# Performance work log

Measured on AMD Instinct MI355X. Metric: run time of the kernel, lower is better.

Reference implementation:

```python
import jax, jax.numpy as jnp
import numpy as np

B, T, D = 256, 64, 512          # batch, seq_len, enc_input_size == dec_output_size
HE, L = 1024, 512               # enc_hidden_size, latent == con_hidden == dec_hidden
BAR, BAR_UNITS = 4, 16          # conductor bars, steps per bar (BAR*BAR_UNITS == T)


def _lstm_step(x, h, c, Wih, Whh, bih, bhh):
    # torch LSTM gate order: i, f, g, o
    g = x @ Wih.T + bih + h @ Whh.T + bhh
    i, f, gg, o = jnp.split(g, 4, axis=-1)
    c = jax.nn.sigmoid(f) * c + jax.nn.sigmoid(i) * jnp.tanh(gg)
    h = jax.nn.sigmoid(o) * jnp.tanh(c)
    return h, c


def _run_lstm_final_h(x_t, Wih, Whh, bih, bhh):
    # x_t: (T, B, D_in); returns final hidden state (B, H)
    Bb = x_t.shape[1]
    H = Whh.shape[1]
    init = (jnp.zeros((Bb, H), x_t.dtype), jnp.zeros((Bb, H), x_t.dtype))
    def step(carry, xt):
        h, c = _lstm_step(xt, carry[0], carry[1], Wih, Whh, bih, bhh)
        return (h, c), None
    (h, _), _ = jax.lax.scan(step, init, x_t)
    return h


def reference(x, eps, We_ih_f, We_hh_f, be_ih_f, be_hh_f, We_ih_b, We_hh_b, be_ih_b, be_hh_b,
              Wmu, bmu, Wstd, bstd, Wc_ih0, Wc_hh0, bc_ih0, bc_hh0, Wc_ih1, Wc_hh1, bc_ih1, bc_hh1,
              Wcl, bcl, Wd_ih0, Wd_hh0, bd_ih0, bd_hh0, Wd_ih1, Wd_hh1, bd_ih1, bd_hh1, Wlog, blog):
    x_t = jnp.transpose(x, (1, 0, 2))  # (T, B, D)
    # ---- Encoder: 1-layer bidirectional LSTM, take final hidden of each direction ----
    h_f = _run_lstm_final_h(x_t, We_ih_f, We_hh_f, be_ih_f, be_hh_f)
    h_b = _run_lstm_final_h(x_t[::-1], We_ih_b, We_hh_b, be_ih_b, be_hh_b)
    henc = jnp.concatenate([h_f, h_b], axis=-1)  # (B, 2*HE)
    mu_raw = henc @ Wmu.T + bmu
    mu = (mu_raw - mu_raw.mean(-1, keepdims=True)) / jnp.sqrt(mu_raw.var(-1, keepdims=True) + 1e-5)
    std = jax.nn.softplus(henc @ Wstd.T + bstd)
    z = mu + eps * std  # (B, L)
    # ---- Conductor: 2-layer LSTM, h0=c0=z, input is z at every bar step ----
    h0 = c0 = h1 = c1 = z
    feats = []
    for _ in range(BAR):
        h0, c0 = _lstm_step(z, h0, c0, Wc_ih0, Wc_hh0, bc_ih0, bc_hh0)
        h1, c1 = _lstm_step(h0, h1, c1, Wc_ih1, Wc_hh1, bc_ih1, bc_hh1)
        feats.append(h1)
    feat = jnp.stack(feats, axis=1) @ Wcl.T + bcl  # (B, BAR, L)
    # ---- Decoder: 2-layer LSTM, teacher-forced, hidden reset to bar embedding each bar ----
    z_t = jnp.transpose(jnp.repeat(feat, BAR_UNITS, axis=1), (1, 0, 2))  # (T, B, L)
    x_prev_t = jnp.concatenate([jnp.zeros((1, x.shape[0], D), x.dtype), x_t[:-1]], axis=0)
    reset_t = (jnp.arange(T) % BAR_UNITS) == 0
    zH = jnp.zeros((x.shape[0], L), x.dtype)
    def dec_step(carry, inp):
        hd1, cd1, hd2, cd2 = carry
        xp, zb, rs = inp
        hd1 = jnp.where(rs, zb, hd1); cd1 = jnp.where(rs, zb, cd1)
        hd2 = jnp.where(rs, zb, hd2); cd2 = jnp.where(rs, zb, cd2)
        xin = jnp.concatenate([xp, zb], axis=-1)  # (B, D+L)
        hd1, cd1 = _lstm_step(xin, hd1, cd1, Wd_ih0, Wd_hh0, bd_ih0, bd_hh0)
        hd2, cd2 = _lstm_step(hd1, hd2, cd2, Wd_ih1, Wd_hh1, bd_ih1, bd_hh1)
        logits = hd2 @ Wlog.T + blog  # temp == 1
        return (hd1, cd1, hd2, cd2), logits
    _, logits_t = jax.lax.scan(dec_step, (zH, zH, zH, zH), (x_prev_t, z_t, reset_t))
    prob = jnp.transpose(jax.nn.softmax(logits_t, axis=-1), (1, 0, 2))  # (B, T, D)
    label = jnp.argmax(prob, axis=-1).astype(jnp.float32)  # (B, T)
    return prob, mu, std, label


def setup_inputs() -> dict:
    key = jax.random.key(0)
    ks = iter(jax.random.split(key, 40))
    def w(shape, fan):
        return jax.random.normal(next(ks), shape, jnp.float32) * (1.0 / np.sqrt(fan))
    return {
        'x': jax.random.normal(next(ks), (B, T, D), jnp.float32),
        'eps': jax.random.normal(next(ks), (B, L), jnp.float32),
        'We_ih_f': w((4 * HE, D), HE), 'We_hh_f': w((4 * HE, HE), HE),
        'be_ih_f': w((4 * HE,), HE), 'be_hh_f': w((4 * HE,), HE),
        'We_ih_b': w((4 * HE, D), HE), 'We_hh_b': w((4 * HE, HE), HE),
        'be_ih_b': w((4 * HE,), HE), 'be_hh_b': w((4 * HE,), HE),
        'Wmu': w((L, 2 * HE), 2 * HE), 'bmu': w((L,), 2 * HE),
        'Wstd': w((L, 2 * HE), 2 * HE), 'bstd': w((L,), 2 * HE),
        'Wc_ih0': w((4 * L, L), L), 'Wc_hh0': w((4 * L, L), L),
        'bc_ih0': w((4 * L,), L), 'bc_hh0': w((4 * L,), L),
        'Wc_ih1': w((4 * L, L), L), 'Wc_hh1': w((4 * L, L), L),
        'bc_ih1': w((4 * L,), L), 'bc_hh1': w((4 * L,), L),
        'Wcl': w((L, L), L), 'bcl': w((L,), L),
        'Wd_ih0': w((4 * L, L + D), L), 'Wd_hh0': w((4 * L, L), L),
        'bd_ih0': w((4 * L,), L), 'bd_hh0': w((4 * L,), L),
        'Wd_ih1': w((4 * L, L), L), 'Wd_hh1': w((4 * L, L), L),
        'bd_ih1': w((4 * L,), L), 'bd_hh1': w((4 * L,), L),
        'Wlog': w((D, L), L), 'blog': w((D,), L),
    }
```

## Files before the change

### kernel.cpp

```cpp
#include <hip/hip_runtime.h>
#include <cstddef>
#include <cstdint>

static constexpr int B  = 256;
static constexpr int T  = 64;
static constexpr int D  = 512;
static constexpr int HE = 1024;
static constexpr int L  = 512;

typedef unsigned short ushort_t;
typedef __attribute__((ext_vector_type(8))) short short8;
typedef __attribute__((ext_vector_type(8))) _Float16 f16x8;
typedef __attribute__((ext_vector_type(4))) float f32x4;
typedef __attribute__((ext_vector_type(4))) unsigned short ushort4_t;

static constexpr float LO_SCALE   = 2048.0f;
static constexpr float LO_UNSCALE = 4.8828125e-4f;

__device__ __forceinline__ float sigmoidf_(float x) { return 1.0f / (1.0f + expf(-x)); }

struct hfp { ushort_t hi, lo; };
__device__ __forceinline__ hfp f16_split(float v) {
    _Float16 h = (_Float16)v;
    _Float16 l = (_Float16)((v - (float)h) * LO_SCALE);
    hfp r;
    r.hi = __builtin_bit_cast(ushort_t, h);
    r.lo = __builtin_bit_cast(ushort_t, l);
    return r;
}

__device__ __forceinline__ size_t tile_off(int m, int n, int ldt) {
    return ((size_t)(m >> 4) * ldt + (n >> 5)) * 512
         + (size_t)((((m & 15) + (((n >> 3) & 3) << 4)) << 3) + (n & 7));
}

__global__ void pack_w(const float* __restrict__ src, ushort_t* __restrict__ hi,
                       ushort_t* __restrict__ lo, int Np, int K, int H)
{
    int idx = blockIdx.x * 256 + threadIdx.x;
    int pc = K >> 2;
    if (idx >= Np * pc) return;
    int p = idx / pc, kc = (idx - p * pc) << 2;
    int srow = p;
    if (H) srow = ((p >> 4) & 3) * H + (p >> 6) * 16 + (p & 15);
    float4 v = *(const float4*)(src + (size_t)srow * K + kc);
    ushort4_t h, l;
    hfp a;
    a = f16_split(v.x); h[0] = a.hi; l[0] = a.lo;
    a = f16_split(v.y); h[1] = a.hi; l[1] = a.lo;
    a = f16_split(v.z); h[2] = a.hi; l[2] = a.lo;
    a = f16_split(v.w); h[3] = a.hi; l[3] = a.lo;
    size_t off = tile_off(p, kc, K >> 5);
    *(ushort4_t*)(hi + off) = h;
    *(ushort4_t*)(lo + off) = l;
}

__global__ void pack_bias(const float* __restrict__ b1, const float* __restrict__ b2,
                          float* __restrict__ dst, int H)
{
    int p = blockIdx.x * 256 + threadIdx.x;
    if (p >= 4 * H) return;
    int srow = ((p >> 4) & 3) * H + (p >> 6) * 16 + (p & 15);
    dst[p] = b1[srow] + b2[srow];
}

__global__ void conv_x(const float* __restrict__ x, ushort_t* __restrict__ xh,
                       ushort_t* __restrict__ xl)
{
    int idx = blockIdx.x * 256 + threadIdx.x;
    if (idx >= T * B * D / 4) return;
    int r = idx >> 7;
    int kc = (idx & 127) << 2;
    int t = r >> 8, b = r & 255;
    float4 v = *(const float4*)(x + ((size_t)b * T + t) * D + kc);
    ushort4_t h, l;
    hfp a;
    a = f16_split(v.x); h[0] = a.hi; l[0] = a.lo;
    a = f16_split(v.y); h[1] = a.hi; l[1] = a.lo;
    a = f16_split(v.z); h[2] = a.hi; l[2] = a.lo;
    a = f16_split(v.w); h[3] = a.hi; l[3] = a.lo;
    size_t off = (size_t)t * B * D + tile_off(b, kc, D >> 5);
    *(ushort4_t*)(xh + off) = h;
    *(ushort4_t*)(xl + off) = l;
}

struct Op {
    const ushort_t *Ahi, *Alo; int ldtA, kt0A;
    const ushort_t *Whi, *Wlo; int ldtW, kt0W;
    int K;
};
struct MArgs {
    Op op[3];
    const float* ci0; int ld0;
    int mode;
    const float* cin; int cinLd;
    float* cout; int coutLd;
    ushort_t *hHi, *hLo; int hLdT;
    float* out; int outLd;
    ushort_t *pHi, *pLo; int pLdT;
};

__device__ __forceinline__ f32x4 MFH(short8 a, short8 w, f32x4 c) {
    return __builtin_amdgcn_mfma_f32_16x16x32_f16(
        __builtin_bit_cast(f16x8, a), __builtin_bit_cast(f16x8, w), c, 0, 0, 0);
}

template<int TAG>
__global__ __launch_bounds__(256) void gemm_sk(MArgs ga0, MArgs ga1)
{
    __shared__ float LV[4][2][4][4][64];
    const MArgs& ga = blockIdx.z ? ga1 : ga0;
    const int tid  = threadIdx.x;
    const int lane = tid & 63;
    const int wk   = tid >> 6;
    const int m_w = blockIdx.y * 32;
    const int n_w = blockIdx.x * 64;
    const int l15 = lane & 15;

    f32x4 accH[2][4], accL[2][4];
#pragma unroll
    for (int mf = 0; mf < 2; ++mf)
#pragma unroll
        for (int j = 0; j < 4; ++j)
#pragma unroll
            for (int r = 0; r < 4; ++r) { accH[mf][j][r] = 0.0f; accL[mf][j][r] = 0.0f; }

    int NT = 0;
#pragma unroll
    for (int opi = 0; opi < 3; ++opi)
        if (ga.op[opi].Ahi && ga.op[opi].K > 0) NT += ga.op[opi].K >> 5;
    const int share = NT >> 2;
    int skip = wk * share, cnt = share;

#pragma unroll 1
    for (int opi = 0; opi < 3 && cnt > 0; ++opi) {
        const Op o = ga.op[opi];
        if (o.Ahi == nullptr || o.K <= 0) continue;
        const int NK = o.K >> 5;
        if (skip >= NK) { skip -= NK; continue; }
        const int k0 = skip;
        const int k1 = (NK - k0 < cnt) ? NK : k0 + cnt;
        cnt -= (k1 - k0);
        skip = 0;

        const ushort_t *aHp[2], *aLp[2], *wHp[4], *wLp[4];
#pragma unroll
        for (int mf = 0; mf < 2; ++mf) {
            size_t ro = ((size_t)((m_w >> 4) + mf) * o.ldtA + o.kt0A) * 512 + lane * 8;
            aHp[mf] = o.Ahi + ro; aLp[mf] = o.Alo + ro;
        }
#pragma unroll
        for (int j = 0; j < 4; ++j) {
            size_t ro = ((size_t)((n_w >> 4) + j) * o.ldtW + o.kt0W) * 512 + lane * 8;
            wHp[j] = o.Whi + ro; wLp[j] = o.Wlo + ro;
        }

        short8 A0[2], L0[2], W0[4], V0[4];
        short8 A1[2], L1[2], W1[4], V1[4];
        auto LD0 = [&](int ks) {
#pragma unroll
            for (int mf = 0; mf < 2; ++mf) {
                A0[mf] = *(const short8*)(aHp[mf] + (size_t)ks * 512);
                L0[mf] = *(const short8*)(aLp[mf] + (size_t)ks * 512);
            }
#pragma unroll
            for (int j = 0; j < 4; ++j) {
                W0[j] = *(const short8*)(wHp[j] + (size_t)ks * 512);
                V0[j] = *(const short8*)(wLp[j] + (size_t)ks * 512);
            }
        };
        auto LD1 = [&](int ks) {
#pragma unroll
            for (int mf = 0; mf < 2; ++mf) {
                A1[mf] = *(const short8*)(aHp[mf] + (size_t)ks * 512);
                L1[mf] = *(const short8*)(aLp[mf] + (size_t)ks * 512);
            }
#pragma unroll
            for (int j = 0; j < 4; ++j) {
                W1[j] = *(const short8*)(wHp[j] + (size_t)ks * 512);
                V1[j] = *(const short8*)(wLp[j] + (size_t)ks * 512);
            }
        };
        auto MM0 = [&]() {
#pragma unroll
            for (int mf = 0; mf < 2; ++mf)
#pragma unroll
                for (int j = 0; j < 4; ++j) {
                    accL[mf][j] = MFH(A0[mf], V0[j], accL[mf][j]);
                    accL[mf][j] = MFH(L0[mf], W0[j], accL[mf][j]);
                    accH[mf][j] = MFH(A0[mf], W0[j], accH[mf][j]);
                }
        };
        auto MM1 = [&]() {
#pragma unroll
            for (int mf = 0; mf < 2; ++mf)
#pragma unroll
                for (int j = 0; j < 4; ++j) {
                    accL[mf][j] = MFH(A1[mf], V1[j], accL[mf][j]);
                    accL[mf][j] = MFH(L1[mf], W1[j], accL[mf][j]);
                    accH[mf][j] = MFH(A1[mf], W1[j], accH[mf][j]);
                }
        };

        LD0(k0);
        int ks = k0;
        for (; ks + 2 < k1; ks += 2) {
            LD1(ks + 1);
            MM0();
            LD0(ks + 2);
            MM1();
        }
        if (ks + 1 < k1) { LD1(ks + 1); MM0(); MM1(); }
        else MM0();
    }

#pragma unroll
    for (int mf = 0; mf < 2; ++mf)
#pragma unroll
        for (int j = 0; j < 4; ++j)
#pragma unroll
            for (int r = 0; r < 4; ++r)
                LV[wk][mf][j][r][lane] = accH[mf][j][r] + LO_UNSCALE * accL[mf][j][r];
    __syncthreads();

    const int mf = wk >> 1;
    const int rb = (wk & 1) * 2;
#pragma unroll
    for (int rr = 0; rr < 2; ++rr) {
        const int r = rb + rr;
        float g[4];
#pragma unroll
        for (int j = 0; j < 4; ++j) {
            float s = 0.0f;
#pragma unroll
            for (int w2 = 0; w2 < 4; ++w2) s += LV[w2][mf][j][r][lane];
            if (ga.ci0) s += ga.ci0[n_w + j * 16 + l15];
            g[j] = s;
        }
        const int m = m_w + mf * 16 + (lane >> 4) * 4 + r;
        if (ga.mode == 1) {
            const int n = (n_w >> 6) * 16 + l15;
            const float cold = ga.cin[(size_t)m * ga.cinLd + n];
            const float cn = sigmoidf_(g[1]) * cold + sigmoidf_(g[0]) * tanhf(g[2]);
            const float h  = sigmoidf_(g[3]) * tanhf(cn);
            ga.cout[(size_t)m * ga.coutLd + n] = cn;
            hfp hp = f16_split(h);
            size_t off = tile_off(m, n, ga.hLdT);
            ga.hHi[off] = hp.hi;
            ga.hLo[off] = hp.lo;
        } else {
#pragma unroll
            for (int j = 0; j < 4; ++j) {
                const int p = n_w + j * 16 + l15;
                int dst = m;
                if (ga.mode == 2) dst = ((m & (B - 1)) << 6) + (m >> 8);
                if (ga.out) ga.out[(size_t)dst * ga.outLd + p] = g[j];
                if (ga.pHi) {
                    hfp vp = f16_split(g[j]);
                    size_t off = tile_off(m, p, ga.pLdT);
                    ga.pHi[off] = vp.hi;
                    ga.pLo[off] = vp.lo;
                }
            }
        }
    }
}

template<int TAG, int MF, int WM, int WN>
__global__ __launch_bounds__(WM * WN * 64) void gemm_t(MArgs ga0, MArgs ga1)
{
    const MArgs& ga = blockIdx.z ? ga1 : ga0;
    const int lane = threadIdx.x & 63;
    const int wid  = threadIdx.x >> 6;
    const int wy = wid / WN, wx = wid % WN;
    const int m_w = blockIdx.y * (WM * MF * 16) + wy * MF * 16;
    const int n_w = blockIdx.x * (WN * 64) + wx * 64;
    const int l15 = lane & 15;
    const int rB  = (lane >> 4) * 4;

    f32x4 accH[MF][4];
    f32x4 accL[MF][4];
#pragma unroll
    for (int mf = 0; mf < MF; ++mf)
#pragma unroll
        for (int j = 0; j < 4; ++j) {
            const int p = n_w + j * 16 + l15;
#pragma unroll
            for (int r = 0; r < 4; ++r) {
                float v = 0.0f;
                if (ga.ci0) v += ga.ci0[(size_t)(m_w + mf * 16 + rB + r) * ga.ld0 + p];
                accH[mf][j][r] = v;
                accL[mf][j][r] = 0.0f;
            }
        }

#pragma unroll 1
    for (int opi = 0; opi < 3; ++opi) {
        const Op o = ga.op[opi];
        if (o.Ahi == nullptr || o.K <= 0) continue;
        const ushort_t *aH[MF], *aL[MF], *wH[4], *wL[4];
#pragma unroll
        for (int mf = 0; mf < MF; ++mf) {
            size_t ro = ((size_t)((m_w >> 4) + mf) * o.ldtA + o.kt0A) * 512 + lane * 8;
            aH[mf] = o.Ahi + ro; aL[mf] = o.Alo + ro;
        }
#pragma unroll
        for (int j = 0; j < 4; ++j) {
            size_t ro = ((size_t)((n_w >> 4) + j) * o.ldtW + o.kt0W) * 512 + lane * 8;
            wH[j] = o.Whi + ro; wL[j] = o.Wlo + ro;
        }
        const int NK = o.K >> 5;

        auto LD = [&](short8* ah, short8* al, short8* wh, short8* wl, int ks) {
#pragma unroll
            for (int mf = 0; mf < MF; ++mf) {
                ah[mf] = *(const short8*)(aH[mf] + (size_t)ks * 512);
                al[mf] = *(const short8*)(aL[mf] + (size_t)ks * 512);
            }
#pragma unroll
            for (int j = 0; j < 4; ++j) {
                wh[j] = *(const short8*)(wH[j] + (size_t)ks * 512);
                wl[j] = *(const short8*)(wL[j] + (size_t)ks * 512);
            }
        };
        auto MM = [&](short8* ah, short8* al, short8* wh, short8* wl) {
#pragma unroll
            for (int mf = 0; mf < MF; ++mf)
#pragma unroll
                for (int j = 0; j < 4; ++j) {
                    accL[mf][j] = MFH(ah[mf], wl[j], accL[mf][j]);
                    accL[mf][j] = MFH(al[mf], wh[j], accL[mf][j]);
                    accH[mf][j] = MFH(ah[mf], wh[j], accH[mf][j]);
                }
        };

        short8 A0[MF], L0[MF], W0[4], V0[4];
        short8 A1[MF], L1[MF], W1[4], V1[4];
        LD(A0, L0, W0, V0, 0);
        int ks = 0;
        for (; ks + 2 < NK; ks += 2) {
            LD(A1, L1, W1, V1, ks + 1);
            MM(A0, L0, W0, V0);
            LD(A0, L0, W0, V0, ks + 2);
            MM(A1, L1, W1, V1);
        }
        LD(A1, L1, W1, V1, ks + 1);
        MM(A0, L0, W0, V0);
        MM(A1, L1, W1, V1);
    }

    if (ga.mode == 1) {
        const int n = (n_w >> 6) * 16 + l15;
#pragma unroll
        for (int mf = 0; mf < MF; ++mf)
#pragma unroll
            for (int r = 0; r < 4; ++r) {
                const int m = m_w + mf * 16 + rB + r;
                const float gi = accH[mf][0][r] + LO_UNSCALE * accL[mf][0][r];
                const float gf = accH[mf][1][r] + LO_UNSCALE * accL[mf][1][r];
                const float gg = accH[mf][2][r] + LO_UNSCALE * accL[mf][2][r];
                const float go = accH[mf][3][r] + LO_UNSCALE * accL[mf][3][r];
                const float cold = ga.cin[(size_t)m * ga.cinLd + n];
                const float cn = sigmoidf_(gf) * cold + sigmoidf_(gi) * tanhf(gg);
                const float h  = sigmoidf_(go) * tanhf(cn);
                ga.cout[(size_t)m * ga.coutLd + n] = cn;
                hfp hp = f16_split(h);
                size_t off = tile_off(m, n, ga.hLdT);
                ga.hHi[off] = hp.hi;
                ga.hLo[off] = hp.lo;
            }
    } else {
#pragma unroll
        for (int mf = 0; mf < MF; ++mf)
#pragma unroll
            for (int j = 0; j < 4; ++j) {
                const int p = n_w + j * 16 + l15;
#pragma unroll
                for (int r = 0; r < 4; ++r) {
                    const int m = m_w + mf * 16 + rB + r;
                    const float v = accH[mf][j][r] + LO_UNSCALE * accL[mf][j][r];
                    int dst = m;
                    if (ga.mode == 2) dst = ((m & (B - 1)) << 6) + (m >> 8);
                    if (ga.out) ga.out[(size_t)dst * ga.outLd + p] = v;
                    if (ga.pHi) {
                        hfp vp = f16_split(v);
                        size_t off = tile_off(m, p, ga.pLdT);
                        ga.pHi[off] = vp.hi;
                        ga.pLo[off] = vp.lo;
                    }
                }
            }
    }
}

__global__ void latent2(float* __restrict__ mu, float* __restrict__ sd,
                        const float* __restrict__ eps, float* __restrict__ c0,
                        float* __restrict__ c1, ushort_t* __restrict__ zh,
                        ushort_t* __restrict__ zl)
{
    const int b = blockIdx.x, l = threadIdx.x;
    float* mrow = mu + (size_t)b * L;
    float4 v0 = *(const float4*)(mrow + l * 4);
    float4 v1 = *(const float4*)(mrow + 256 + l * 4);
    float s = v0.x + v0.y + v0.z + v0.w + v1.x + v1.y + v1.z + v1.w;
    float q = v0.x * v0.x + v0.y * v0.y + v0.z * v0.z + v0.w * v0.w
            + v1.x * v1.x + v1.y * v1.y + v1.z * v1.z + v1.w * v1.w;
#pragma unroll
    for (int off = 32; off; off >>= 1) { s += __shfl_xor(s, off); q += __shfl_xor(q, off); }
    const float mean = s * (1.0f / 512.0f);
    const float var  = q * (1.0f / 512.0f) - mean * mean;
    const float inv  = rsqrtf(var + 1e-5f);
    v0.x = (v0.x - mean) * inv; v0.y = (v0.y - mean) * inv; v0.z = (v0.z - mean) * inv; v0.w = (v0.w - mean) * inv;
    v1.x = (v1.x - mean) * inv; v1.y = (v1.y - mean) * inv; v1.z = (v1.z - mean) * inv; v1.w = (v1.w - mean) * inv;
    *(float4*)(mrow + l * 4) = v0;
    *(float4*)(mrow + 256 + l * 4) = v1;

    float* srow = sd + (size_t)b * L;
    float4 s0 = *(const float4*)(srow + l * 4);
    float4 s1 = *(const float4*)(srow + 256 + l * 4);
    s0.x = fmaxf(s0.x, 0.0f) + log1pf(expf(-fabsf(s0.x)));
    s0.y = fmaxf(s0.y, 0.0f) + log1pf(expf(-fabsf(s0.y)));
    s0.z = fmaxf(s0.z, 0.0f) + log1pf(expf(-fabsf(s0.z)));
    s0.w = fmaxf(s0.w, 0.0f) + log1pf(expf(-fabsf(s0.w)));
    s1.x = fmaxf(s1.x, 0.0f) + log1pf(expf(-fabsf(s1.x)));
    s1.y = fmaxf(s1.y, 0.0f) + log1pf(expf(-fabsf(s1.y)));
    s1.z = fmaxf(s1.z, 0.0f) + log1pf(expf(-fabsf(s1.z)));
    s1.w = fmaxf(s1.w, 0.0f) + log1pf(expf(-fabsf(s1.w)));
    *(float4*)(srow + l * 4) = s0;
    *(float4*)(srow + 256 + l * 4) = s1;

    const float* erow = eps + (size_t)b * L;
    float4 e0 = *(const float4*)(erow + l * 4);
    float4 e1 = *(const float4*)(erow + 256 + l * 4);
    float4 z0, z1;
    z0.x = v0.x + e0.x * s0.x; z0.y = v0.y + e0.y * s0.y; z0.z = v0.z + e0.z * s0.z; z0.w = v0.w + e0.w * s0.w;
    z1.x = v1.x + e1.x * s1.x; z1.y = v1.y + e1.y * s1.y; z1.z = v1.z + e1.z * s1.z; z1.w = v1.w + e1.w * s1.w;
    *(float4*)(c0 + (size_t)b * L + l * 4) = z0;
    *(float4*)(c0 + (size_t)b * L + 256 + l * 4) = z1;
    *(float4*)(c1 + (size_t)b * L + l * 4) = z0;
    *(float4*)(c1 + (size_t)b * L + 256 + l * 4) = z1;
    ushort4_t h, lo;
    hfp a;
    a = f16_split(z0.x); h[0] = a.hi; lo[0] = a.lo;
    a = f16_split(z0.y); h[1] = a.hi; lo[1] = a.lo;
    a = f16_split(z0.z); h[2] = a.hi; lo[2] = a.lo;
    a = f16_split(z0.w); h[3] = a.hi; lo[3] = a.lo;
    size_t o0 = tile_off(b, l * 4, 16);
    *(ushort4_t*)(zh + o0) = h;
    *(ushort4_t*)(zl + o0) = lo;
    a = f16_split(z1.x); h[0] = a.hi; lo[0] = a.lo;
    a = f16_split(z1.y); h[1] = a.hi; lo[1] = a.lo;
    a = f16_split(z1.z); h[2] = a.hi; lo[2] = a.lo;
    a = f16_split(z1.w); h[3] = a.hi; lo[3] = a.lo;
    size_t o1 = tile_off(b, 256 + l * 4, 16);
    *(ushort4_t*)(zh + o1) = h;
    *(ushort4_t*)(zl + o1) = lo;
}

__global__ void softmax_all(float* __restrict__ prob, float* __restrict__ label)
{
    const int r = blockIdx.x, l = threadIdx.x;
    float* row = prob + (size_t)r * D;
    float4 x0 = *(const float4*)(row + l * 4);
    float4 x1 = *(const float4*)(row + 256 + l * 4);
    float m = x0.x; int mi = l * 4;
    { float v; int i;
      v = x0.y; i = l * 4 + 1;       if (v > m) { m = v; mi = i; }
      v = x0.z; i = l * 4 + 2;       if (v > m) { m = v; mi = i; }
      v = x0.w; i = l * 4 + 3;       if (v > m) { m = v; mi = i; }
      v = x1.x; i = 256 + l * 4;     if (v > m) { m = v; mi = i; }
      v = x1.y; i = 256 + l * 4 + 1; if (v > m) { m = v; mi = i; }
      v = x1.z; i = 256 + l * 4 + 2; if (v > m) { m = v; mi = i; }
      v = x1.w; i = 256 + l * 4 + 3; if (v > m) { m = v; mi = i; } }
#pragma unroll
    for (int off = 32; off; off >>= 1) {
        float om = __shfl_xor(m, off);
        int   oi = __shfl_xor(mi, off);
        if (om > m || (om == m && oi < mi)) { m = om; mi = oi; }
    }
    float4 e0, e1;
    e0.x = expf(x0.x - m); e0.y = expf(x0.y - m); e0.z = expf(x0.z - m); e0.w = expf(x0.w - m);
    e1.x = expf(x1.x - m); e1.y = expf(x1.y - m); e1.z = expf(x1.z - m); e1.w = expf(x1.w - m);
    float s = e0.x + e0.y + e0.z + e0.w + e1.x + e1.y + e1.z + e1.w;
#pragma unroll
    for (int off = 32; off; off >>= 1) s += __shfl_xor(s, off);
    const float inv = 1.0f / s;
    e0.x *= inv; e0.y *= inv; e0.z *= inv; e0.w *= inv;
    e1.x *= inv; e1.y *= inv; e1.z *= inv; e1.w *= inv;
    *(float4*)(row + l * 4) = e0;
    *(float4*)(row + 256 + l * 4) = e1;
    if (l == 0) label[r] = (float)mi;
}

extern "C" void kernel_launch(void* const* d_in, const int* in_sizes, int n_in,
                              void* d_out, int out_size, void* d_ws, size_t ws_size,
                              hipStream_t stream)
{
    const float* x       = (const float*)d_in[0];
    const float* eps     = (const float*)d_in[1];
    const float* We_ih_f = (const float*)d_in[2];
    const float* We_hh_f = (const float*)d_in[3];
    const float* be_ih_f = (const float*)d_in[4];
    const float* be_hh_f = (const float*)d_in[5];
    const float* We_ih_b = (const float*)d_in[6];
    const float* We_hh_b = (const float*)d_in[7];
    const float* be_ih_b = (const float*)d_in[8];
    const float* be_hh_b = (const float*)d_in[9];
    const float* Wmu     = (const float*)d_in[10];
    const float* bmu     = (const float*)d_in[11];
    const float* Wstd    = (const float*)d_in[12];
    const float* bstd    = (const float*)d_in[13];
    const float* Wc_ih0  = (const float*)d_in[14];
    const float* Wc_hh0  = (const float*)d_in[15];
    const float* bc_ih0  = (const float*)d_in[16];
    const float* bc_hh0  = (const float*)d_in[17];
    const float* Wc_ih1  = (const float*)d_in[18];
    const float* Wc_hh1  = (const float*)d_in[19];
    const float* bc_ih1  = (const float*)d_in[20];
    const float* bc_hh1  = (const float*)d_in[21];
    const float* Wcl     = (const float*)d_in[22];
    const float* bcl     = (const float*)d_in[23];
    const float* Wd_ih0  = (const float*)d_in[24];
    const float* Wd_hh0  = (const float*)d_in[25];
    const float* bd_ih0  = (const float*)d_in[26];
    const float* bd_hh0  = (const float*)d_in[27];
    const float* Wd_ih1  = (const float*)d_in[28];
    const float* Wd_hh1  = (const float*)d_in[29];
    const float* bd_ih1  = (const float*)d_in[30];
    const float* bd_hh1  = (const float*)d_in[31];
    const float* Wlog    = (const float*)d_in[32];
    const float* blog    = (const float*)d_in[33];
    (void)in_sizes; (void)n_in; (void)out_size;

    float* out      = (float*)d_out;
    float* prob_out = out;
    float* mu_out   = out + (size_t)B * T * D;
    float* std_out  = mu_out + (size_t)B * L;
    float* lab_out  = std_out + (size_t)B * L;

    char* cur = (char*)d_ws;
    auto alignup = [&]() { cur = (char*)(((uintptr_t)cur + 255) & ~(uintptr_t)255); };
    auto aU = [&](size_t elems) { alignup(); ushort_t* p = (ushort_t*)cur; cur += elems * 2; return p; };
    auto aF = [&](size_t elems) { alignup(); float* p = (float*)cur; cur += elems * 4; return p; };

    ushort_t* WefIh = aU((size_t)4*HE*D);  ushort_t* WefIl = aU((size_t)4*HE*D);
    ushort_t* WefHh = aU((size_t)4*HE*HE); ushort_t* WefHl = aU((size_t)4*HE*HE);
    ushort_t* WebIh = aU((size_t)4*HE*D);  ushort_t* WebIl = aU((size_t)4*HE*D);
    ushort_t* WebHh = aU((size_t)4*HE*HE); ushort_t* WebHl = aU((size_t)4*HE*HE);
    ushort_t* Wc0Ih = aU((size_t)4*L*L);   ushort_t* Wc0Il = aU((size_t)4*L*L);
    ushort_t* Wc0Hh = aU((size_t)4*L*L);   ushort_t* Wc0Hl = aU((size_t)4*L*L);
    ushort_t* Wc1Ih = aU((size_t)4*L*L);   ushort_t* Wc1Il = aU((size_t)4*L*L);
    ushort_t* Wc1Hh = aU((size_t)4*L*L);   ushort_t* Wc1Hl = aU((size_t)4*L*L);
    ushort_t* Wd0Ih = aU((size_t)4*L*(D+L)); ushort_t* Wd0Il = aU((size_t)4*L*(D+L));
    ushort_t* Wd0Hh = aU((size_t)4*L*L);   ushort_t* Wd0Hl = aU((size_t)4*L*L);
    ushort_t* Wd1Ih = aU((size_t)4*L*L);   ushort_t* Wd1Il = aU((size_t)4*L*L);
    ushort_t* Wd1Hh = aU((size_t)4*L*L);   ushort_t* Wd1Hl = aU((size_t)4*L*L);
    ushort_t* WmuH  = aU((size_t)L*2*HE);  ushort_t* WmuL  = aU((size_t)L*2*HE);
    ushort_t* WstdH = aU((size_t)L*2*HE);  ushort_t* WstdL = aU((size_t)L*2*HE);
    ushort_t* WclH  = aU((size_t)L*L);     ushort_t* WclL  = aU((size_t)L*L);
    ushort_t* WlogH = aU((size_t)D*L);     ushort_t* WlogL = aU((size_t)D*L);
    ushort_t* xh = aU((size_t)T*B*D);      ushort_t* xl = aU((size_t)T*B*D);
    ushort_t* hfh[2] = { aU((size_t)B*HE), aU((size_t)B*HE) };
    ushort_t* hfl[2] = { aU((size_t)B*HE), aU((size_t)B*HE) };
    ushort_t* hbh[2] = { aU((size_t)B*HE), aU((size_t)B*HE) };
    ushort_t* hbl[2] = { aU((size_t)B*HE), aU((size_t)B*HE) };
    ushort_t* zh = aU((size_t)B*L);        ushort_t* zl = aU((size_t)B*L);
    ushort_t* h0h[2] = { aU((size_t)B*L), aU((size_t)B*L) };
    ushort_t* h0l[2] = { aU((size_t)B*L), aU((size_t)B*L) };
    ushort_t* ftsH = aU((size_t)4*B*L);    ushort_t* ftsL = aU((size_t)4*B*L);
    ushort_t* featH = aU((size_t)4*B*L);   ushort_t* featL = aU((size_t)4*B*L);
    ushort_t* hd1h[2] = { aU((size_t)B*L), aU((size_t)B*L) };
    ushort_t* hd1l[2] = { aU((size_t)B*L), aU((size_t)B*L) };
    ushort_t* slabH = aU((size_t)T*B*L);   ushort_t* slabL = aU((size_t)T*B*L);
    float* cf   = aF((size_t)B*HE);
    float* cb   = aF((size_t)B*HE);
    float* zbuf = aF((size_t)B*HE);
    float* c0   = aF((size_t)B*L);
    float* c1   = aF((size_t)B*L);
    float* cd1  = aF((size_t)B*L);
    float* cd2  = aF((size_t)B*L);
    float* featF = aF((size_t)4*B*L);
    float* bEF = aF((size_t)4*HE);
    float* bEB = aF((size_t)4*HE);
    float* bC0 = aF((size_t)4*L);
    float* bC1 = aF((size_t)4*L);
    float* bD0 = aF((size_t)4*L);
    float* bD1 = aF((size_t)4*L);
    const size_t need = (size_t)(cur - (char*)d_ws);
    if (need > ws_size) return;

    auto PK = [&](const float* s, ushort_t* h, ushort_t* l, int Np, int K, int H) {
        int tot = Np * (K >> 2);
        pack_w<<<(tot + 255) / 256, 256, 0, stream>>>(s, h, l, Np, K, H);
    };
    PK(We_ih_f, WefIh, WefIl, 4*HE, D, HE);
    PK(We_hh_f, WefHh, WefHl, 4*HE, HE, HE);
    PK(We_ih_b, WebIh, WebIl, 4*HE, D, HE);
    PK(We_hh_b, WebHh, WebHl, 4*HE, HE, HE);
    PK(Wc_ih0, Wc0Ih, Wc0Il, 4*L, L, L);
    PK(Wc_hh0, Wc0Hh, Wc0Hl, 4*L, L, L);
    PK(Wc_ih1, Wc1Ih, Wc1Il, 4*L, L, L);
    PK(Wc_hh1, Wc1Hh, Wc1Hl, 4*L, L, L);
    PK(Wd_ih0, Wd0Ih, Wd0Il, 4*L, D+L, L);
    PK(Wd_hh0, Wd0Hh, Wd0Hl, 4*L, L, L);
    PK(Wd_ih1, Wd1Ih, Wd1Il, 4*L, L, L);
    PK(Wd_hh1, Wd1Hh, Wd1Hl, 4*L, L, L);
    PK(Wmu,  WmuH,  WmuL,  L, 2*HE, 0);
    PK(Wstd, WstdH, WstdL, L, 2*HE, 0);
    PK(Wcl,  WclH,  WclL,  L, L, 0);
    PK(Wlog, WlogH, WlogL, D, L, 0);
    pack_bias<<<(4*HE + 255) / 256, 256, 0, stream>>>(be_ih_f, be_hh_f, bEF, HE);
    pack_bias<<<(4*HE + 255) / 256, 256, 0, stream>>>(be_ih_b, be_hh_b, bEB, HE);
    pack_bias<<<(4*L + 255) / 256, 256, 0, stream>>>(bc_ih0, bc_hh0, bC0, L);
    pack_bias<<<(4*L + 255) / 256, 256, 0, stream>>>(bc_ih1, bc_hh1, bC1, L);
    pack_bias<<<(4*L + 255) / 256, 256, 0, stream>>>(bd_ih0, bd_hh0, bD0, L);
    pack_bias<<<(4*L + 255) / 256, 256, 0, stream>>>(bd_ih1, bd_hh1, bD1, L);
    conv_x<<<(T*B*D/4 + 255) / 256, 256, 0, stream>>>(x, xh, xl);
    (void)hipMemsetAsync(zbuf, 0, (size_t)B * HE * sizeof(float), stream);

    for (int t = 0; t < T; ++t) {
        MArgs f{};
        f.op[0] = { xh + (size_t)t*B*D, xl + (size_t)t*B*D, 16, 0, WefIh, WefIl, 16, 0, D };
        if (t) f.op[1] = { hfh[t&1], hfl[t&1], 32, 0, WefHh, WefHl, 32, 0, HE };
        f.ci0 = bEF; f.ld0 = 0;
        f.mode = 1;
        f.cin = t ? cf : zbuf; f.cinLd = HE;
        f.cout = cf; f.coutLd = HE;
        f.hHi = hfh[(t+1)&1]; f.hLo = hfl[(t+1)&1]; f.hLdT = 32;
        MArgs b = f;
        b.op[0] = { xh + (size_t)(T-1-t)*B*D, xl + (size_t)(T-1-t)*B*D, 16, 0, WebIh, WebIl, 16, 0, D };
        if (t) b.op[1] = { hbh[t&1], hbl[t&1], 32, 0, WebHh, WebHl, 32, 0, HE };
        b.ci0 = bEB;
        b.cin = t ? cb : zbuf;
        b.cout = cb;
        b.hHi = hbh[(t+1)&1]; b.hLo = hbl[(t+1)&1];
        gemm_sk<0><<<dim3(4*HE/64, B/32, 2), 256, 0, stream>>>(f, b);
    }

    {
        MArgs m{};
        m.op[0] = { hfh[0], hfl[0], 32, 0, WmuH, WmuL, 64, 0, HE };
        m.op[1] = { hbh[0], hbl[0], 32, 0, WmuH, WmuL, 64, 32, HE };
        m.ci0 = bmu; m.ld0 = 0; m.mode = 0; m.out = mu_out; m.outLd = L;
        MArgs s = m;
        s.op[0].Whi = WstdH; s.op[0].Wlo = WstdL;
        s.op[1].Whi = WstdH; s.op[1].Wlo = WstdL;
        s.ci0 = bstd; s.out = std_out;
        gemm_t<3,1,1,1><<<dim3(L/64, B/16, 2), 64, 0, stream>>>(m, s);
        latent2<<<B, 64, 0, stream>>>(mu_out, std_out, eps, c0, c1, zh, zl);
    }

    auto condL1 = [&](int bar) {
        MArgs a{};
        a.op[0] = { zh, zl, 16, 0, Wc0Ih, Wc0Il, 16, 0, L };
        a.op[1] = { bar ? h0h[(bar-1)&1] : zh, bar ? h0l[(bar-1)&1] : zl, 16, 0, Wc0Hh, Wc0Hl, 16, 0, L };
        a.ci0 = bC0; a.ld0 = 0; a.mode = 1;
        a.cin = c0; a.cinLd = L; a.cout = c0; a.coutLd = L;
        a.hHi = h0h[bar&1]; a.hLo = h0l[bar&1]; a.hLdT = 16;
        return a;
    };
    auto condL2 = [&](int bar) {
        MArgs a2{};
        a2.op[0] = { h0h[bar&1], h0l[bar&1], 16, 0, Wc1Ih, Wc1Il, 16, 0, L };
        if (bar) a2.op[1] = { ftsH + (size_t)(bar-1)*B*L, ftsL + (size_t)(bar-1)*B*L, 16, 0, Wc1Hh, Wc1Hl, 16, 0, L };
        else     a2.op[1] = { zh, zl, 16, 0, Wc1Hh, Wc1Hl, 16, 0, L };
        a2.ci0 = bC1; a2.ld0 = 0; a2.mode = 1;
        a2.cin = c1; a2.cinLd = L; a2.cout = c1; a2.coutLd = L;
        a2.hHi = ftsH + (size_t)bar*B*L; a2.hLo = ftsL + (size_t)bar*B*L; a2.hLdT = 16;
        return a2;
    };
    {
        MArgs l1 = condL1(0);
        gemm_sk<2><<<dim3(4*L/64, B/32, 1), 256, 0, stream>>>(l1, l1);
        for (int bar = 0; bar < 4; ++bar) {
            MArgs l2 = condL2(bar);
            if (bar + 1 < 4) {
                MArgs n1 = condL1(bar + 1);
                gemm_sk<2><<<dim3(4*L/64, B/32, 2), 256, 0, stream>>>(l2, n1);
            } else {
                gemm_sk<2><<<dim3(4*L/64, B/32, 1), 256, 0, stream>>>(l2, l2);
            }
        }
    }
    {
        MArgs af{};
        af.op[0] = { ftsH, ftsL, 16, 0, WclH, WclL, 16, 0, L };
        af.ci0 = bcl; af.ld0 = 0; af.mode = 0;
        af.out = featF; af.outLd = L;
        af.pHi = featH; af.pLo = featL; af.pLdT = 16;
        gemm_t<3,1,1,1><<<dim3(L/64, 4*B/16, 1), 64, 0, stream>>>(af, af);
    }

    auto decG1 = [&](int t) {
        const int bar = t >> 4;
        const bool rs = (t & 15) == 0;
        MArgs g1{};
        if (t) g1.op[0] = { xh + (size_t)(t-1)*B*D, xl + (size_t)(t-1)*B*D, 16, 0, Wd0Ih, Wd0Il, 32, 0, D };
        g1.op[1] = { featH + (size_t)bar*B*L, featL + (size_t)bar*B*L, 16, 0, Wd0Ih, Wd0Il, 32, 16, L };
        if (rs) g1.op[2] = { featH + (size_t)bar*B*L, featL + (size_t)bar*B*L, 16, 0, Wd0Hh, Wd0Hl, 16, 0, L };
        else    g1.op[2] = { hd1h[(t-1)&1], hd1l[(t-1)&1], 16, 0, Wd0Hh, Wd0Hl, 16, 0, L };
        g1.ci0 = bD0; g1.ld0 = 0; g1.mode = 1;
        g1.cin = rs ? featF + (size_t)bar*B*L : cd1; g1.cinLd = L;
        g1.cout = cd1; g1.coutLd = L;
        g1.hHi = hd1h[t&1]; g1.hLo = hd1l[t&1]; g1.hLdT = 16;
        return g1;
    };
    auto decG2 = [&](int t) {
        const int bar = t >> 4;
        const bool rs = (t & 15) == 0;
        MArgs g2{};
        g2.op[0] = { hd1h[t&1], hd1l[t&1], 16, 0, Wd1Ih, Wd1Il, 16, 0, L };
        if (rs) g2.op[1] = { featH + (size_t)bar*B*L, featL + (size_t)bar*B*L, 16, 0, Wd1Hh, Wd1Hl, 16, 0, L };
        else    g2.op[1] = { slabH + (size_t)(t-1)*B*L, slabL + (size_t)(t-1)*B*L, 16, 0, Wd1Hh, Wd1Hl, 16, 0, L };
        g2.ci0 = bD1; g2.ld0 = 0; g2.mode = 1;
        g2.cin = rs ? featF + (size_t)bar*B*L : cd2; g2.cinLd = L;
        g2.cout = cd2; g2.coutLd = L;
        g2.hHi = slabH + (size_t)t*B*L; g2.hLo = slabL + (size_t)t*B*L; g2.hLdT = 16;
        return g2;
    };
    {
        MArgs g1 = decG1(0);
        gemm_sk<4><<<dim3(4*L/64, B/32, 1), 256, 0, stream>>>(g1, g1);
        for (int t = 0; t < T; ++t) {
            MArgs g2 = decG2(t);
            if (t + 1 < T) {
                MArgs n1 = decG1(t + 1);
                gemm_sk<4><<<dim3(4*L/64, B/32, 2), 256, 0, stream>>>(g2, n1);
            } else {
                gemm_sk<4><<<dim3(4*L/64, B/32, 1), 256, 0, stream>>>(g2, g2);
            }
        }
    }

    {
        MArgs lg{};
        lg.op[0] = { slabH, slabL, 16, 0, WlogH, WlogL, 16, 0, L };
        lg.ci0 = blog; lg.ld0 = 0; lg.mode = 2;
        lg.out = prob_out; lg.outLd = D;
        gemm_t<5,2,2,2><<<dim3(D/128, T*B/64, 1), 256, 0, stream>>>(lg, lg);
    }
    softmax_all<<<B * T, 64, 0, stream>>>(prob_out, lab_out);
}
```

Baseline: 3.634 ms.

## Precompute decoder layer-1 input projections outside the recurrent loop

Moves the teacher-forced x projection and the bar-feature projection of decoder layer 1 out of the per-step recurrent GEMM. They are now computed as batched GEMMs per bar, for 16 timesteps at once, plus one feature GEMM for all bars. Each step then only does the hidden-to-hidden matmul and adds the precomputed rows through new per-row bias inputs (ci0/ci1 with row strides). This shortens the serial critical path of the decoder. In exchange it needs extra workspace, which falls back to the old path if the workspace is too small, and adds bulk GEMM launches plus an initfix kernel that sets up step 0.

After: 6.332 ms. 1.74x slower.

```diff
diff --git a/kernel.cpp b/kernel.cpp
--- a/kernel.cpp
+++ b/kernel.cpp
@@ -84,6 +84,13 @@
     *(ushort4_t*)(xl + off) = l;
 }
 
+__global__ void initfix(float* __restrict__ dst, const float* __restrict__ b)
+{
+    int idx = blockIdx.x * 256 + threadIdx.x;
+    if (idx >= 256 * 2048) return;
+    dst[idx] = b[idx & 2047];
+}
+
 struct Op {
     const ushort_t *Ahi, *Alo; int ldtA, kt0A;
     const ushort_t *Whi, *Wlo; int ldtW, kt0W;
@@ -92,6 +99,7 @@
 struct MArgs {
     Op op[3];
     const float* ci0; int ld0;
+    const float* ci1; int ld1;
     int mode;
     const float* cin; int cinLd;
     float* cout; int coutLd;
@@ -105,11 +113,9 @@
         __builtin_bit_cast(f16x8, a), __builtin_bit_cast(f16x8, w), c, 0, 0, 0);
 }
 
-template<int TAG>
-__global__ __launch_bounds__(256) void gemm_sk(MArgs ga0, MArgs ga1)
+__device__ __forceinline__ void sk_body(const MArgs& ga)
 {
     __shared__ float LV[4][2][4][4][64];
-    const MArgs& ga = blockIdx.z ? ga1 : ga0;
     const int tid  = threadIdx.x;
     const int lane = tid & 63;
     const int wk   = tid >> 6;
@@ -228,16 +234,18 @@
 #pragma unroll
     for (int rr = 0; rr < 2; ++rr) {
         const int r = rb + rr;
+        const int m = m_w + mf * 16 + (lane >> 4) * 4 + r;
         float g[4];
 #pragma unroll
         for (int j = 0; j < 4; ++j) {
             float s = 0.0f;
 #pragma unroll
             for (int w2 = 0; w2 < 4; ++w2) s += LV[w2][mf][j][r][lane];
-            if (ga.ci0) s += ga.ci0[n_w + j * 16 + l15];
+            const int p = n_w + j * 16 + l15;
+            if (ga.ci0) s += ga.ci0[ga.ld0 ? (size_t)m * ga.ld0 + p : (size_t)p];
+            if (ga.ci1) s += ga.ci1[ga.ld1 ? (size_t)m * ga.ld1 + p : (size_t)p];
             g[j] = s;
         }
-        const int m = m_w + mf * 16 + (lane >> 4) * 4 + r;
         if (ga.mode == 1) {
             const int n = (n_w >> 6) * 16 + l15;
             const float cold = ga.cin[(size_t)m * ga.cinLd + n];
@@ -266,10 +274,13 @@
     }
 }
 
-template<int TAG, int MF, int WM, int WN>
-__global__ __launch_bounds__(WM * WN * 64) void gemm_t(MArgs ga0, MArgs ga1)
-{
-    const MArgs& ga = blockIdx.z ? ga1 : ga0;
+__global__ __launch_bounds__(256) void enc_sk(MArgs a, MArgs b) { sk_body(blockIdx.z ? b : a); }
+__global__ __launch_bounds__(256) void cond_sk(MArgs a, MArgs b) { sk_body(blockIdx.z ? b : a); }
+__global__ __launch_bounds__(256) void dec_sk(MArgs a, MArgs b) { sk_body(blockIdx.z ? b : a); }
+
+template<int MF, int WM, int WN>
+__device__ __forceinline__ void t_body(const MArgs& ga)
+{
     const int lane = threadIdx.x & 63;
     const int wid  = threadIdx.x >> 6;
     const int wy = wid / WN, wx = wid % WN;
@@ -288,7 +299,7 @@
 #pragma unroll
             for (int r = 0; r < 4; ++r) {
                 float v = 0.0f;
-                if (ga.ci0) v += ga.ci0[(size_t)(m_w + mf * 16 + rB + r) * ga.ld0 + p];
+                if (ga.ci0) v += ga.ci0[ga.ld0 ? (size_t)(m_w + mf * 16 + rB + r) * ga.ld0 + p : (size_t)p];
                 accH[mf][j][r] = v;
                 accL[mf][j][r] = 0.0f;
             }
@@ -392,6 +403,12 @@
             }
     }
 }
+
+__global__ __launch_bounds__(64)  void lat_t(MArgs a, MArgs b)  { t_body<1,1,1>(blockIdx.z ? b : a); }
+__global__ __launch_bounds__(64)  void feat_t(MArgs a, MArgs b) { t_body<1,1,1>(blockIdx.z ? b : a); }
+__global__ __launch_bounds__(256) void log_t(MArgs a, MArgs b)  { t_body<2,2,2>(blockIdx.z ? b : a); }
+__global__ __launch_bounds__(256) void pre_t(MArgs a, MArgs b)  { t_body<2,2,2>(blockIdx.z ? b : a); }
+__global__ __launch_bounds__(256) void fin_t(MArgs a, MArgs b)  { t_body<2,2,2>(blockIdx.z ? b : a); }
 
 __global__ void latent2(float* __restrict__ mu, float* __restrict__ sd,
                         const float* __restrict__ eps, float* __restrict__ c0,
@@ -586,8 +603,11 @@
     float* bC1 = aF((size_t)4*L);
     float* bD0 = aF((size_t)4*L);
     float* bD1 = aF((size_t)4*L);
-    const size_t need = (size_t)(cur - (char*)d_ws);
-    if (need > ws_size) return;
+    const size_t need_base = (size_t)(cur - (char*)d_ws);
+    if (need_base > ws_size) return;
+    float* g1init = aF((size_t)16*B*4*L);
+    float* fInit  = aF((size_t)4*B*4*L);
+    const bool pre = ((size_t)(cur - (char*)d_ws) <= ws_size);
 
     auto PK = [&](const float* s, ushort_t* h, ushort_t* l, int Np, int K, int H) {
         int tot = Np * (K >> 2);
@@ -634,7 +654,7 @@
         b.cin = t ? cb : zbuf;
         b.cout = cb;
         b.hHi = hbh[(t+1)&1]; b.hLo = hbl[(t+1)&1];
-        gemm_sk<0><<<dim3(4*HE/64, B/32, 2), 256, 0, stream>>>(f, b);
+        enc_sk<<<dim3(4*HE/64, B/32, 2), 256, 0, stream>>>(f, b);
     }
 
     {
@@ -646,7 +666,7 @@
         s.op[0].Whi = WstdH; s.op[0].Wlo = WstdL;
         s.op[1].Whi = WstdH; s.op[1].Wlo = WstdL;
         s.ci0 = bstd; s.out = std_out;
-        gemm_t<3,1,1,1><<<dim3(L/64, B/16, 2), 64, 0, stream>>>(m, s);
+        lat_t<<<dim3(L/64, B/16, 2), 64, 0, stream>>>(m, s);
         latent2<<<B, 64, 0, stream>>>(mu_out, std_out, eps, c0, c1, zh, zl);
     }
 
@@ -671,14 +691,14 @@
     };
     {
         MArgs l1 = condL1(0);
-        gemm_sk<2><<<dim3(4*L/64, B/32, 1), 256, 0, stream>>>(l1, l1);
+        cond_sk<<<dim3(4*L/64, B/32, 1), 256, 0, stream>>>(l1, l1);
         for (int bar = 0; bar < 4; ++bar) {
             MArgs l2 = condL2(bar);
             if (bar + 1 < 4) {
                 MArgs n1 = condL1(bar + 1);
-                gemm_sk<2><<<dim3(4*L/64, B/32, 2), 256, 0, stream>>>(l2, n1);
+                cond_sk<<<dim3(4*L/64, B/32, 2), 256, 0, stream>>>(l2, n1);
             } else {
-                gemm_sk<2><<<dim3(4*L/64, B/32, 1), 256, 0, stream>>>(l2, l2);
+                cond_sk<<<dim3(4*L/64, B/32, 1), 256, 0, stream>>>(l2, l2);
             }
         }
     }
@@ -688,18 +708,43 @@
         af.ci0 = bcl; af.ld0 = 0; af.mode = 0;
         af.out = featF; af.outLd = L;
         af.pHi = featH; af.pLo = featL; af.pLdT = 16;
-        gemm_t<3,1,1,1><<<dim3(L/64, 4*B/16, 1), 64, 0, stream>>>(af, af);
-    }
+        feat_t<<<dim3(L/64, 4*B/16, 1), 64, 0, stream>>>(af, af);
+    }
+
+    if (pre) {
+        MArgs fi{};
+        fi.op[0] = { featH, featL, 16, 0, Wd0Ih, Wd0Il, 32, 16, L };
+        fi.mode = 0; fi.out = fInit; fi.outLd = 4*L;
+        fin_t<<<dim3(4*L/128, 4*B/64, 1), 256, 0, stream>>>(fi, fi);
+    }
+    auto xpart = [&](int bar) {
+        MArgs px{};
+        px.op[0] = { xh + ((size_t)(bar*16) - 1) * B * D, xl + ((size_t)(bar*16) - 1) * B * D,
+                     16, 0, Wd0Ih, Wd0Il, 32, 0, D };
+        px.ci0 = bD0; px.ld0 = 0;
+        px.mode = 0; px.out = g1init; px.outLd = 4*L;
+        pre_t<<<dim3(4*L/128, 16*B/64, 1), 256, 0, stream>>>(px, px);
+        if (bar == 0)
+            initfix<<<(256*2048)/256, 256, 0, stream>>>(g1init, bD0);
+    };
 
     auto decG1 = [&](int t) {
         const int bar = t >> 4;
         const bool rs = (t & 15) == 0;
         MArgs g1{};
-        if (t) g1.op[0] = { xh + (size_t)(t-1)*B*D, xl + (size_t)(t-1)*B*D, 16, 0, Wd0Ih, Wd0Il, 32, 0, D };
-        g1.op[1] = { featH + (size_t)bar*B*L, featL + (size_t)bar*B*L, 16, 0, Wd0Ih, Wd0Il, 32, 16, L };
-        if (rs) g1.op[2] = { featH + (size_t)bar*B*L, featL + (size_t)bar*B*L, 16, 0, Wd0Hh, Wd0Hl, 16, 0, L };
-        else    g1.op[2] = { hd1h[(t-1)&1], hd1l[(t-1)&1], 16, 0, Wd0Hh, Wd0Hl, 16, 0, L };
-        g1.ci0 = bD0; g1.ld0 = 0; g1.mode = 1;
+        if (pre) {
+            if (rs) g1.op[0] = { featH + (size_t)bar*B*L, featL + (size_t)bar*B*L, 16, 0, Wd0Hh, Wd0Hl, 16, 0, L };
+            else    g1.op[0] = { hd1h[(t-1)&1], hd1l[(t-1)&1], 16, 0, Wd0Hh, Wd0Hl, 16, 0, L };
+            g1.ci0 = g1init + (size_t)(t & 15) * B * 4*L; g1.ld0 = 4*L;
+            g1.ci1 = fInit + (size_t)bar * B * 4*L;       g1.ld1 = 4*L;
+        } else {
+            if (t) g1.op[0] = { xh + (size_t)(t-1)*B*D, xl + (size_t)(t-1)*B*D, 16, 0, Wd0Ih, Wd0Il, 32, 0, D };
+            g1.op[1] = { featH + (size_t)bar*B*L, featL + (size_t)bar*B*L, 16, 0, Wd0Ih, Wd0Il, 32, 16, L };
+            if (rs) g1.op[2] = { featH + (size_t)bar*B*L, featL + (size_t)bar*B*L, 16, 0, Wd0Hh, Wd0Hl, 16, 0, L };
+            else    g1.op[2] = { hd1h[(t-1)&1], hd1l[(t-1)&1], 16, 0, Wd0Hh, Wd0Hl, 16, 0, L };
+            g1.ci0 = bD0; g1.ld0 = 0;
+        }
+        g1.mode = 1;
         g1.cin = rs ? featF + (size_t)bar*B*L : cd1; g1.cinLd = L;
         g1.cout = cd1; g1.coutLd = L;
         g1.hHi = hd1h[t&1]; g1.hLo = hd1l[t&1]; g1.hLdT = 16;
@@ -719,15 +764,17 @@
         return g2;
     };
     {
+        if (pre) xpart(0);
         MArgs g1 = decG1(0);
-        gemm_sk<4><<<dim3(4*L/64, B/32, 1), 256, 0, stream>>>(g1, g1);
+        dec_sk<<<dim3(4*L/64, B/32, 1), 256, 0, stream>>>(g1, g1);
         for (int t = 0; t < T; ++t) {
+            if (pre && ((t + 1) & 15) == 0 && t + 1 < T) xpart((t + 1) >> 4);
             MArgs g2 = decG2(t);
             if (t + 1 < T) {
                 MArgs n1 = decG1(t + 1);
-                gemm_sk<4><<<dim3(4*L/64, B/32, 2), 256, 0, stream>>>(g2, n1);
+                dec_sk<<<dim3(4*L/64, B/32, 2), 256, 0, stream>>>(g2, n1);
             } else {
-                gemm_sk<4><<<dim3(4*L/64, B/32, 1), 256, 0, stream>>>(g2, g2);
+                dec_sk<<<dim3(4*L/64, B/32, 1), 256, 0, stream>>>(g2, g2);
             }
         }
     }
@@ -737,7 +784,7 @@
         lg.op[0] = { slabH, slabL, 16, 0, WlogH, WlogL, 16, 0, L };
         lg.ci0 = blog; lg.ld0 = 0; lg.mode = 2;
         lg.out = prob_out; lg.outLd = D;
-        gemm_t<5,2,2,2><<<dim3(D/128, T*B/64, 1), 256, 0, stream>>>(lg, lg);
+        log_t<<<dim3(D/128, T*B/64, 1), 256, 0, stream>>>(lg, lg);
     }
     softmax_all<<<B * T, 64, 0, stream>>>(prob_out, lab_out);
 }
```
